# Performance work log

Hardware: AMD Instinct MI355X
Metric: run time of the kernel (lower is better)

## Reference

```python
import jax, jax.numpy as jnp
import numpy as np

N_HEAD = 8


def setup_inputs() -> dict:
    key = jax.random.key(0)
    k1, k2, k3 = jax.random.split(key, 3)
    B, D, L = 4, 1024, 2048  # channels-first: (batch, feature, seq)
    q = jax.random.normal(k1, (B, D, L), dtype=jnp.float32)
    k = jax.random.normal(k2, (B, D, L), dtype=jnp.float32)
    v = jax.random.normal(k3, (B, D, L), dtype=jnp.float32)
    gamma = jnp.ones((), dtype=jnp.float32)  # nn.Parameter scalar, init 1.0
    return {"q": q, "k": k, "v": v, "gamma": gamma}


def reference(q, k, v, gamma):
    # q, k, v: (B, D, L) channels-first. Head split on feature dim (-2).
    B, Dq, Lq = q.shape
    Dv, Lk = v.shape[-2], v.shape[-1]
    h = N_HEAD
    dq = Dq // h  # per-head query/key dim
    dv = Dv // h  # per-head value dim
    qh = q.reshape(B, h, dq, Lq)
    kh = k.reshape(B, h, dq, Lk)
    vh = v.reshape(B, h, dv, Lk)
    # scale = sqrt(q.size(-2)) AFTER head split, i.e. sqrt(d_head)
    scale = 1.0 / jnp.sqrt(jnp.asarray(dq, dtype=q.dtype))
    # qk: (B, h, Lq, Lk)
    qk = jnp.einsum('bhdq,bhdl->bhql', qh, kh) * scale
    sm = jax.nn.softmax(qk, axis=-1)
    # torch: (sm.unsqueeze(-3) * v.unsqueeze(-2)).sum(-1) == contraction over Lk
    ret = jnp.einsum('bhql,bhdl->bhdq', sm, vh)  # (B, h, dv, Lq)
    ret = ret.reshape(B, Dv, Lq)  # torch: ret.view(-1, v_shape[-2], q_shape[-1])
    return gamma * ret
```

## Files before the change

### kernel.cpp

```cpp
#include <hip/hip_runtime.h>

#define SEQ 2048
#define DHEAD 128
#define BK 32
#define NBH 32

typedef __attribute__((ext_vector_type(8))) short bf16x8;
typedef __attribute__((ext_vector_type(4))) float f32x4;

__device__ __forceinline__ unsigned short f2bf(float f) {
    unsigned u = __builtin_bit_cast(unsigned, f);
    u += 0x7fffu + ((u >> 16) & 1u);
    return (unsigned short)(u >> 16);
}

__device__ __forceinline__ void gload16(const unsigned short* g, unsigned short* l) {
    __builtin_amdgcn_global_load_lds((const __attribute__((address_space(1))) void*)g,
                                     (__attribute__((address_space(3))) void*)l, 16, 0, 0);
}

__global__ __launch_bounds__(256)
void cvt_kernel(const float* __restrict__ kin, const float* __restrict__ vin,
                unsigned short* __restrict__ kout, unsigned short* __restrict__ vout) {
    const int tid = threadIdx.x;
    if (blockIdx.x < 1024) {
        __shared__ unsigned short tileT[DHEAD][66];
        const int bh = blockIdx.x & 31;
        const int l0 = (blockIdx.x >> 5) * 64;
        const float* ip = kin + (size_t)bh * DHEAD * SEQ;
        unsigned short* opx = kout + ((size_t)bh * SEQ + l0) * DHEAD;
        const int l4 = (tid & 15) * 4;
        const int dq = tid >> 4;
        for (int pass = 0; pass < 8; ++pass) {
            int d = pass * 16 + dq;
            float4 f = *(const float4*)&ip[(size_t)d * SEQ + l0 + l4];
            unsigned lo = (unsigned)f2bf(f.x) | ((unsigned)f2bf(f.y) << 16);
            unsigned hi = (unsigned)f2bf(f.z) | ((unsigned)f2bf(f.w) << 16);
            *(unsigned*)&tileT[d][l4]     = lo;
            *(unsigned*)&tileT[d][l4 + 2] = hi;
        }
        __syncthreads();
        const int lw = tid >> 2;
        const int cw = tid & 3;
        for (int j = 0; j < 4; ++j) {
            int pc = j * 4 + cw;
            int lc = pc ^ (lw & 7);
            unsigned short tmp[8];
            for (int k2 = 0; k2 < 8; ++k2) tmp[k2] = tileT[lc * 8 + k2][lw];
            *(bf16x8*)&opx[(size_t)lw * DHEAD + pc * 8] = *(bf16x8*)tmp;
        }
    } else {
        size_t f = ((size_t)(blockIdx.x - 1024) * 256 + tid) * 8;
        int bh  = (int)(f >> 18);
        int rem = (int)(f & 262143);
        int kt  = rem >> 12;
        int r2  = rem & 4095;
        int dv  = r2 >> 5;
        int e0  = r2 & 31;
        const float* src = vin + ((size_t)bh * DHEAD + dv) * SEQ + kt * BK + e0;
        float4 a = *(const float4*)src;
        float4 b = *(const float4*)(src + 4);
        unsigned short r[8] = {f2bf(a.x), f2bf(a.y), f2bf(a.z), f2bf(a.w),
                               f2bf(b.x), f2bf(b.y), f2bf(b.z), f2bf(b.w)};
        int pc = (e0 >> 3) ^ ((dv >> 1) & 3);
        size_t off = ((size_t)bh * (SEQ / BK) + kt) * (DHEAD * BK) + dv * BK + pc * 8;
        *(bf16x8*)&vout[off] = *(bf16x8*)r;
    }
}

__global__ __launch_bounds__(256, 1)
void attn_main(const float* __restrict__ q,
               const unsigned short* __restrict__ kTg,
               const unsigned short* __restrict__ vW,
               const float* __restrict__ gamma,
               float* __restrict__ out) {
    __shared__ unsigned short kS[2][BK * DHEAD];
    __shared__ unsigned short vS[2][DHEAD * BK];
    __shared__ unsigned short pS[4][16][40];

    const int tid  = threadIdx.x;
    const int wv   = tid >> 6;
    const int lane = tid & 63;
    const int c    = lane & 15;
    const int quad = lane >> 4;

    const int bh  = blockIdx.x & 31;
    const int qlb = blockIdx.x >> 5;
    const size_t base = (size_t)bh * SEQ * DHEAD;

    const float* qp = q + base;
    const unsigned short* kb = kTg + base;
    const unsigned short* vb = vW + base;
    float* op = out + base;

    const int ql0 = qlb * 256 + wv * 64;
    const float SCL = 0.08838834764831845f * 1.44269504088896340f;

    bf16x8 qf[4][4];
    for (int rs = 0; rs < 4; ++rs) {
        const int ql = ql0 + rs * 16 + c;
        for (int s = 0; s < 4; ++s) {
            bf16x8 fqs;
            for (int j = 0; j < 8; ++j)
                fqs[j] = (short)f2bf(qp[(size_t)(s * 32 + quad * 8 + j) * SEQ + ql] * SCL);
            qf[rs][s] = fqs;
        }
    }

    f32x4 accO[4][8];
    for (int rs = 0; rs < 4; ++rs)
        for (int t = 0; t < 8; ++t)
            accO[rs][t] = (f32x4){0.f, 0.f, 0.f, 0.f};
    float lp[4][4];
    for (int rs = 0; rs < 4; ++rs)
        for (int r = 0; r < 4; ++r) lp[rs][r] = 0.f;

    const int ksw = c & 7;
    const int vsw = (c >> 1) & 3;

    {
        gload16(kb + tid * 8,         &kS[0][tid * 8]);
        gload16(kb + (tid + 256) * 8, &kS[0][(tid + 256) * 8]);
        gload16(vb + tid * 8,         &vS[0][tid * 8]);
        gload16(vb + (tid + 256) * 8, &vS[0][(tid + 256) * 8]);
    }

    for (int kt = 0; kt < SEQ / BK; ++kt) {
        const int cur = kt & 1;
        __syncthreads();

        if (kt + 1 < SEQ / BK) {
            const unsigned short* kg = kb + (size_t)(kt + 1) * (BK * DHEAD);
            gload16(kg + tid * 8,         &kS[cur ^ 1][tid * 8]);
            gload16(kg + (tid + 256) * 8, &kS[cur ^ 1][(tid + 256) * 8]);
            const unsigned short* vg = vb + (size_t)(kt + 1) * (DHEAD * BK);
            gload16(vg + tid * 8,         &vS[cur ^ 1][tid * 8]);
            gload16(vg + (tid + 256) * 8, &vS[cur ^ 1][(tid + 256) * 8]);
        }

        bf16x8 kf0[4], kf1[4];
        for (int s = 0; s < 4; ++s) {
            int pc = (4 * s + quad) ^ ksw;
            kf0[s] = *(const bf16x8*)&kS[cur][c * DHEAD + pc * 8];
            kf1[s] = *(const bf16x8*)&kS[cur][(16 + c) * DHEAD + pc * 8];
        }
        bf16x8 vf[8];
        for (int t = 0; t < 8; ++t)
            vf[t] = *(const bf16x8*)&vS[cur][(t * 16 + c) * BK + ((quad ^ vsw) * 8)];

        for (int rs = 0; rs < 4; ++rs) {
            f32x4 s0 = (f32x4){0.f, 0.f, 0.f, 0.f};
            f32x4 s1 = (f32x4){0.f, 0.f, 0.f, 0.f};
            for (int s = 0; s < 4; ++s) {
                s0 = __builtin_amdgcn_mfma_f32_16x16x32_bf16(qf[rs][s], kf0[s], s0, 0, 0, 0);
                s1 = __builtin_amdgcn_mfma_f32_16x16x32_bf16(qf[rs][s], kf1[s], s1, 0, 0, 0);
            }

            for (int r = 0; r < 4; ++r) {
                float p0 = exp2f(s0[r]);
                float p1 = exp2f(s1[r]);
                lp[rs][r] += p0 + p1;
                pS[wv][4 * quad + r][c]      = f2bf(p0);
                pS[wv][4 * quad + r][16 + c] = f2bf(p1);
            }
            asm volatile("s_waitcnt lgkmcnt(0)" ::: "memory");

            bf16x8 bp = *(const bf16x8*)&pS[wv][c][quad * 8];
            for (int t = 0; t < 8; ++t)
                accO[rs][t] = __builtin_amdgcn_mfma_f32_16x16x32_bf16(vf[t], bp, accO[rs][t], 0, 0, 0);
        }
    }

    const float gm = gamma[0];
    for (int rs = 0; rs < 4; ++rs) {
        float L[4];
        for (int r = 0; r < 4; ++r) {
            float s = lp[rs][r];
            s += __shfl_xor(s, 1, 16);
            s += __shfl_xor(s, 2, 16);
            s += __shfl_xor(s, 4, 16);
            s += __shfl_xor(s, 8, 16);
            L[r] = s;
        }
        int srcl = (c >> 2) << 4;
        float L0 = __shfl(L[0], srcl);
        float L1 = __shfl(L[1], srcl);
        float L2 = __shfl(L[2], srcl);
        float L3 = __shfl(L[3], srcl);
        int rsel = c & 3;
        float lsel = rsel == 0 ? L0 : rsel == 1 ? L1 : rsel == 2 ? L2 : L3;
        float sc = gm / lsel;
        int ql = ql0 + rs * 16 + c;
        for (int t = 0; t < 8; ++t)
            for (int r = 0; r < 4; ++r)
                op[(size_t)(t * 16 + quad * 4 + r) * SEQ + ql] = accO[rs][t][r] * sc;
    }
}

extern "C" void kernel_launch(void* const* d_in, const int* in_sizes, int n_in,
                              void* d_out, int out_size, void* d_ws, size_t ws_size,
                              hipStream_t stream) {
    (void)in_sizes; (void)n_in; (void)out_size; (void)ws_size;
    const float* q = (const float*)d_in[0];
    const float* k = (const float*)d_in[1];
    const float* v = (const float*)d_in[2];
    const float* g = (const float*)d_in[3];
    float* out = (float*)d_out;

    const size_t PER_T = (size_t)NBH * SEQ * DHEAD;
    unsigned short* kws = (unsigned short*)d_ws;
    unsigned short* vws = kws + PER_T;

    cvt_kernel<<<dim3(1024 + 4096), dim3(256), 0, stream>>>(k, v, kws, vws);
    attn_main<<<dim3(256), dim3(256), 0, stream>>>(q, kws, vws, g, out);
}
```

Baseline: 257.8 us.

## Split key range across waves per block and double the attention grid

Each block now covers 128 queries instead of 256. Two waves per query group each process half of the key sequence, and each wave streams K/V tiles into its own private LDS buffer, so the main loop no longer needs block-wide barriers. The two partial accumulators and row sums are combined through LDS at the end. The grid doubles to 512 blocks with launch bounds allowing two blocks per CU, which is meant to raise occupancy and latency hiding. It also uses a packed bf16 conversion builtin where available; the costs are a final reduction pass, more LDS per block, and a single-buffered per-wave load that may expose load latency.

```diff
diff --git a/kernel.cpp b/kernel.cpp
--- a/kernel.cpp
+++ b/kernel.cpp
@@ -4,6 +4,8 @@
 #define DHEAD 128
 #define BK 32
 #define NBH 32
+#define NKT (SEQ / BK)
+#define HKT (NKT / 2)
 
 typedef __attribute__((ext_vector_type(8))) short bf16x8;
 typedef __attribute__((ext_vector_type(4))) float f32x4;
@@ -12,6 +14,16 @@
     unsigned u = __builtin_bit_cast(unsigned, f);
     u += 0x7fffu + ((u >> 16) & 1u);
     return (unsigned short)(u >> 16);
+}
+
+__device__ __forceinline__ unsigned pack2bf(float a, float b) {
+#if __has_builtin(__builtin_amdgcn_cvt_pk_bf16_f32)
+    typedef __attribute__((ext_vector_type(2))) __bf16 bf16x2_t;
+    bf16x2_t p = __builtin_amdgcn_cvt_pk_bf16_f32(a, b);
+    return __builtin_bit_cast(unsigned, p);
+#else
+    return (unsigned)f2bf(a) | ((unsigned)f2bf(b) << 16);
+#endif
 }
 
 __device__ __forceinline__ void gload16(const unsigned short* g, unsigned short* l) {
@@ -34,10 +46,8 @@
         for (int pass = 0; pass < 8; ++pass) {
             int d = pass * 16 + dq;
             float4 f = *(const float4*)&ip[(size_t)d * SEQ + l0 + l4];
-            unsigned lo = (unsigned)f2bf(f.x) | ((unsigned)f2bf(f.y) << 16);
-            unsigned hi = (unsigned)f2bf(f.z) | ((unsigned)f2bf(f.w) << 16);
-            *(unsigned*)&tileT[d][l4]     = lo;
-            *(unsigned*)&tileT[d][l4 + 2] = hi;
+            *(unsigned*)&tileT[d][l4]     = pack2bf(f.x, f.y);
+            *(unsigned*)&tileT[d][l4 + 2] = pack2bf(f.z, f.w);
         }
         __syncthreads();
         const int lw = tid >> 2;
@@ -60,50 +70,66 @@
         const float* src = vin + ((size_t)bh * DHEAD + dv) * SEQ + kt * BK + e0;
         float4 a = *(const float4*)src;
         float4 b = *(const float4*)(src + 4);
-        unsigned short r[8] = {f2bf(a.x), f2bf(a.y), f2bf(a.z), f2bf(a.w),
-                               f2bf(b.x), f2bf(b.y), f2bf(b.z), f2bf(b.w)};
+        unsigned w0 = pack2bf(a.x, a.y), w1 = pack2bf(a.z, a.w);
+        unsigned w2 = pack2bf(b.x, b.y), w3 = pack2bf(b.z, b.w);
         int pc = (e0 >> 3) ^ ((dv >> 1) & 3);
-        size_t off = ((size_t)bh * (SEQ / BK) + kt) * (DHEAD * BK) + dv * BK + pc * 8;
-        *(bf16x8*)&vout[off] = *(bf16x8*)r;
-    }
-}
-
-__global__ __launch_bounds__(256, 1)
+        size_t off = ((size_t)bh * NKT + kt) * (DHEAD * BK) + dv * BK + pc * 8;
+        uint4 w = {w0, w1, w2, w3};
+        *(bf16x8*)&vout[off] = __builtin_bit_cast(bf16x8, w);
+    }
+}
+
+__global__ __launch_bounds__(256, 2)
 void attn_main(const float* __restrict__ q,
                const unsigned short* __restrict__ kTg,
                const unsigned short* __restrict__ vW,
                const float* __restrict__ gamma,
                float* __restrict__ out) {
-    __shared__ unsigned short kS[2][BK * DHEAD];
-    __shared__ unsigned short vS[2][DHEAD * BK];
+    __shared__ unsigned short kS[4][BK * DHEAD];
+    __shared__ unsigned short vS[4][DHEAD * BK];
     __shared__ unsigned short pS[4][16][40];
+    __shared__ float lred[2][16][64];
 
     const int tid  = threadIdx.x;
     const int wv   = tid >> 6;
     const int lane = tid & 63;
     const int c    = lane & 15;
     const int quad = lane >> 4;
+    const int qg   = wv & 1;
+    const int kh   = wv >> 1;
 
     const int bh  = blockIdx.x & 31;
     const int qlb = blockIdx.x >> 5;
     const size_t base = (size_t)bh * SEQ * DHEAD;
 
     const float* qp = q + base;
-    const unsigned short* kb = kTg + base;
-    const unsigned short* vb = vW + base;
+    const unsigned short* kb = kTg + base + (size_t)(kh * HKT) * (BK * DHEAD);
+    const unsigned short* vb = vW + base + (size_t)(kh * HKT) * (DHEAD * BK);
     float* op = out + base;
 
-    const int ql0 = qlb * 256 + wv * 64;
+    const int ql0 = qlb * 128 + qg * 64;
     const float SCL = 0.08838834764831845f * 1.44269504088896340f;
+
+    const int ksw = c & 7;
+    const int vsw = (c >> 1) & 3;
+
+    for (int ch = 0; ch < 8; ++ch) {
+        gload16(kb + (ch * 64 + lane) * 8, &kS[wv][(ch * 64 + lane) * 8]);
+        gload16(vb + (ch * 64 + lane) * 8, &vS[wv][(ch * 64 + lane) * 8]);
+    }
 
     bf16x8 qf[4][4];
     for (int rs = 0; rs < 4; ++rs) {
         const int ql = ql0 + rs * 16 + c;
         for (int s = 0; s < 4; ++s) {
-            bf16x8 fqs;
-            for (int j = 0; j < 8; ++j)
-                fqs[j] = (short)f2bf(qp[(size_t)(s * 32 + quad * 8 + j) * SEQ + ql] * SCL);
-            qf[rs][s] = fqs;
+            unsigned w0, w1, w2, w3;
+            const float* qc = qp + (size_t)(s * 32 + quad * 8) * SEQ + ql;
+            w0 = pack2bf(qc[0 * SEQ] * SCL, qc[1 * (size_t)SEQ] * SCL);
+            w1 = pack2bf(qc[2 * (size_t)SEQ] * SCL, qc[3 * (size_t)SEQ] * SCL);
+            w2 = pack2bf(qc[4 * (size_t)SEQ] * SCL, qc[5 * (size_t)SEQ] * SCL);
+            w3 = pack2bf(qc[6 * (size_t)SEQ] * SCL, qc[7 * (size_t)SEQ] * SCL);
+            uint4 w = {w0, w1, w2, w3};
+            qf[rs][s] = __builtin_bit_cast(bf16x8, w);
         }
     }
 
@@ -115,38 +141,28 @@
     for (int rs = 0; rs < 4; ++rs)
         for (int r = 0; r < 4; ++r) lp[rs][r] = 0.f;
 
-    const int ksw = c & 7;
-    const int vsw = (c >> 1) & 3;
-
-    {
-        gload16(kb + tid * 8,         &kS[0][tid * 8]);
-        gload16(kb + (tid + 256) * 8, &kS[0][(tid + 256) * 8]);
-        gload16(vb + tid * 8,         &vS[0][tid * 8]);
-        gload16(vb + (tid + 256) * 8, &vS[0][(tid + 256) * 8]);
-    }
-
-    for (int kt = 0; kt < SEQ / BK; ++kt) {
-        const int cur = kt & 1;
-        __syncthreads();
-
-        if (kt + 1 < SEQ / BK) {
-            const unsigned short* kg = kb + (size_t)(kt + 1) * (BK * DHEAD);
-            gload16(kg + tid * 8,         &kS[cur ^ 1][tid * 8]);
-            gload16(kg + (tid + 256) * 8, &kS[cur ^ 1][(tid + 256) * 8]);
-            const unsigned short* vg = vb + (size_t)(kt + 1) * (DHEAD * BK);
-            gload16(vg + tid * 8,         &vS[cur ^ 1][tid * 8]);
-            gload16(vg + (tid + 256) * 8, &vS[cur ^ 1][(tid + 256) * 8]);
-        }
+    for (int i = 0; i < HKT; ++i) {
+        asm volatile("s_waitcnt vmcnt(0)" ::: "memory");
 
         bf16x8 kf0[4], kf1[4];
         for (int s = 0; s < 4; ++s) {
             int pc = (4 * s + quad) ^ ksw;
-            kf0[s] = *(const bf16x8*)&kS[cur][c * DHEAD + pc * 8];
-            kf1[s] = *(const bf16x8*)&kS[cur][(16 + c) * DHEAD + pc * 8];
+            kf0[s] = *(const bf16x8*)&kS[wv][c * DHEAD + pc * 8];
+            kf1[s] = *(const bf16x8*)&kS[wv][(16 + c) * DHEAD + pc * 8];
         }
         bf16x8 vf[8];
         for (int t = 0; t < 8; ++t)
-            vf[t] = *(const bf16x8*)&vS[cur][(t * 16 + c) * BK + ((quad ^ vsw) * 8)];
+            vf[t] = *(const bf16x8*)&vS[wv][(t * 16 + c) * BK + ((quad ^ vsw) * 8)];
+        asm volatile("s_waitcnt lgkmcnt(0)" ::: "memory");
+
+        if (i + 1 < HKT) {
+            const unsigned short* kg = kb + (size_t)(i + 1) * (BK * DHEAD);
+            const unsigned short* vg = vb + (size_t)(i + 1) * (DHEAD * BK);
+            for (int ch = 0; ch < 8; ++ch) {
+                gload16(kg + (ch * 64 + lane) * 8, &kS[wv][(ch * 64 + lane) * 8]);
+                gload16(vg + (ch * 64 + lane) * 8, &vS[wv][(ch * 64 + lane) * 8]);
+            }
+        }
 
         for (int rs = 0; rs < 4; ++rs) {
             f32x4 s0 = (f32x4){0.f, 0.f, 0.f, 0.f};
@@ -155,45 +171,64 @@
                 s0 = __builtin_amdgcn_mfma_f32_16x16x32_bf16(qf[rs][s], kf0[s], s0, 0, 0, 0);
                 s1 = __builtin_amdgcn_mfma_f32_16x16x32_bf16(qf[rs][s], kf1[s], s1, 0, 0, 0);
             }
-
             for (int r = 0; r < 4; ++r) {
                 float p0 = exp2f(s0[r]);
                 float p1 = exp2f(s1[r]);
                 lp[rs][r] += p0 + p1;
-                pS[wv][4 * quad + r][c]      = f2bf(p0);
-                pS[wv][4 * quad + r][16 + c] = f2bf(p1);
+                unsigned pk = pack2bf(p0, p1);
+                pS[wv][4 * quad + r][c]      = (unsigned short)pk;
+                pS[wv][4 * quad + r][16 + c] = (unsigned short)(pk >> 16);
             }
             asm volatile("s_waitcnt lgkmcnt(0)" ::: "memory");
-
             bf16x8 bp = *(const bf16x8*)&pS[wv][c][quad * 8];
             for (int t = 0; t < 8; ++t)
                 accO[rs][t] = __builtin_amdgcn_mfma_f32_16x16x32_bf16(vf[t], bp, accO[rs][t], 0, 0, 0);
         }
     }
 
-    const float gm = gamma[0];
-    for (int rs = 0; rs < 4; ++rs) {
-        float L[4];
-        for (int r = 0; r < 4; ++r) {
-            float s = lp[rs][r];
-            s += __shfl_xor(s, 1, 16);
-            s += __shfl_xor(s, 2, 16);
-            s += __shfl_xor(s, 4, 16);
-            s += __shfl_xor(s, 8, 16);
-            L[r] = s;
-        }
-        int srcl = (c >> 2) << 4;
-        float L0 = __shfl(L[0], srcl);
-        float L1 = __shfl(L[1], srcl);
-        float L2 = __shfl(L[2], srcl);
-        float L3 = __shfl(L[3], srcl);
-        int rsel = c & 3;
-        float lsel = rsel == 0 ? L0 : rsel == 1 ? L1 : rsel == 2 ? L2 : L3;
-        float sc = gm / lsel;
-        int ql = ql0 + rs * 16 + c;
-        for (int t = 0; t < 8; ++t)
+    __syncthreads();
+    float* R = (qg == 0) ? (float*)&kS[0][0] : (float*)&vS[0][0];
+    if (kh == 1) {
+        for (int rs = 0; rs < 4; ++rs) {
+            for (int t = 0; t < 8; ++t)
+                for (int r = 0; r < 4; ++r)
+                    R[((rs * 8 + t) * 4 + r) * 64 + lane] = accO[rs][t][r];
             for (int r = 0; r < 4; ++r)
-                op[(size_t)(t * 16 + quad * 4 + r) * SEQ + ql] = accO[rs][t][r] * sc;
+                lred[qg][rs * 4 + r][lane] = lp[rs][r];
+        }
+    }
+    __syncthreads();
+    if (kh == 0) {
+        const float gm = gamma[0];
+        for (int rs = 0; rs < 4; ++rs) {
+            for (int t = 0; t < 8; ++t)
+                for (int r = 0; r < 4; ++r)
+                    accO[rs][t][r] += R[((rs * 8 + t) * 4 + r) * 64 + lane];
+            for (int r = 0; r < 4; ++r)
+                lp[rs][r] += lred[qg][rs * 4 + r][lane];
+
+            float L[4];
+            for (int r = 0; r < 4; ++r) {
+                float s = lp[rs][r];
+                s += __shfl_xor(s, 1, 16);
+                s += __shfl_xor(s, 2, 16);
+                s += __shfl_xor(s, 4, 16);
+                s += __shfl_xor(s, 8, 16);
+                L[r] = s;
+            }
+            int srcl = (c >> 2) << 4;
+            float L0 = __shfl(L[0], srcl);
+            float L1 = __shfl(L[1], srcl);
+            float L2 = __shfl(L[2], srcl);
+            float L3 = __shfl(L[3], srcl);
+            int rsel = c & 3;
+            float lsel = rsel == 0 ? L0 : rsel == 1 ? L1 : rsel == 2 ? L2 : L3;
+            float sc = gm / lsel;
+            int ql = ql0 + rs * 16 + c;
+            for (int t = 0; t < 8; ++t)
+                for (int r = 0; r < 4; ++r)
+                    op[(size_t)(t * 16 + quad * 4 + r) * SEQ + ql] = accO[rs][t][r] * sc;
+        }
     }
 }
 
@@ -212,5 +247,5 @@
     unsigned short* vws = kws + PER_T;
 
     cvt_kernel<<<dim3(1024 + 4096), dim3(256), 0, stream>>>(k, v, kws, vws);
-    attn_main<<<dim3(256), dim3(256), 0, stream>>>(q, kws, vws, g, out);
-}
+    attn_main<<<dim3(512), dim3(256), 0, stream>>>(q, kws, vws, g, out);
+}
```

Result: slower. 276.1 us (+7.1%).
